# Performance work log

Measured on AMD Instinct MI355X. Metric: run time of the kernel, lower is better.

The kernel has to match this reference:

```python
import jax, jax.numpy as jnp
import numpy as np
import math

C = 16
K = 16
M = 64
DEPTH = 4          # int(sqrt(K)) tree depth
D = C * 9          # input feature dim, 9 dims per codebook subspace
N = 1024 * 128     # rows
N_NODES = K - 1    # 15 internal nodes of a depth-4 binary tree


def _selection_matrix(C):
    # node i at tree level l reads the per-codebook hashed feature at depth index l
    S = np.zeros((C * N_NODES, C * DEPTH), np.float32)
    for c in range(C):
        for i in range(N_NODES):
            level = 0 if i == 0 else (1 if i < 3 else (2 if i < 7 else 3))
            S[c * N_NODES + i, c * DEPTH + level] = 1.0
    return S


def _bit_matrix(C, K):
    # row (c,k): +/-1 on the 4 tree nodes along code k's root-to-leaf path;
    # matching code scores DEPTH, every other code scores <= DEPTH-2
    B = np.zeros((C * K, C * N_NODES), np.float32)
    for c in range(C):
        for k in range(K):
            prefix = 0
            for l in range(DEPTH):
                bit = (k >> (DEPTH - 1 - l)) & 1
                node = (2 ** l - 1) + prefix
                B[c * K + k, c * N_NODES + node] = 1.0 if bit else -1.0
                prefix = prefix * 2 + bit
    return B


def setup_inputs() -> dict:
    key = jax.random.key(0)
    k1, k2, k3, k4 = jax.random.split(key, 4)
    I = jax.random.normal(k1, (N, D), jnp.float32) - 0.5
    A = jax.random.normal(k2, (C, D // C, DEPTH), jnp.float32)   # soft hashing projections
    T = jax.random.normal(k3, (C * N_NODES,), jnp.float32)       # node thresholds
    bound = math.sqrt(1.0 / (C * K))  # kaiming_uniform with a=sqrt(5), fan_in=C*K
    L = jax.random.uniform(k4, (M, C, K), jnp.float32, -bound, bound)  # lookup tables
    S = jnp.asarray(_selection_matrix(C))
    B = jnp.asarray(_bit_matrix(C, K))
    return {"I": I, "A": A, "T": T, "L": L, "S": S, "B": B}


def reference(I, A, T, L, S, B):
    n = I.shape[0]
    # per-codebook soft hash: (n, C, D//C) x (C, D//C, DEPTH) -> (n, C*DEPTH)
    h = jnp.einsum('ncd,cdp->ncp', I.reshape(n, C, D // C), A).reshape(n, C * DEPTH)
    # thresholded tree decisions with straight-through sign
    b = h @ S.T - T                                   # (n, C*15)
    t = jnp.tanh(b)
    s = jax.lax.stop_gradient(jnp.sign(b) - t) + t    # fwd: sign, bwd: tanh'
    # bit-matrix decode of path agreements -> per-code scores
    scores = (s @ B.T).reshape(n, C, K)               # (n, C, K), max DEPTH at true code
    onehot = jax.nn.one_hot(jnp.argmax(scores, axis=2), K, dtype=I.dtype)
    E = jax.lax.stop_gradient(onehot - scores) + scores  # STE one-hot encoding
    # LUT gather-accumulate: out[n,m] = sum_c L[m,c,code(n,c)]
    return jnp.einsum('nck,mck->nm', E, L)
```

## Files before the change

kernel.cpp:

```cpp
#include <hip/hip_runtime.h>


#define NROWS (1024 * 128)

__global__ __launch_bounds__(256) void halut_fwd(
    const float* __restrict__ I,
    const float* __restrict__ A,
    const float* __restrict__ T,
    const float* __restrict__ L,
    float* __restrict__ out)
{
    __shared__ float  sBuf[16384];
    __shared__ double sA[576];
    __shared__ double sT[240];

    const int tid = threadIdx.x;

    {
        float2* sL2 = (float2*)sBuf;
        #pragma unroll
        for (int p2 = 0; p2 < 32; ++p2) {
            const float a = L[(2 * p2)     * 256 + tid];
            const float b = L[(2 * p2 + 1) * 256 + tid];
            sL2[p2 * 256 + tid] = make_float2(a, b);
        }
    }
    for (int i = tid; i < 576; i += 256) sA[i] = (double)A[i];
    if (tid < 240) sT[tid] = (double)T[tid];
    __syncthreads();

    const int    row = blockIdx.x * 256 + tid;
    const float* rp  = I + (size_t)row * 144;

    float acc[64];
    #pragma unroll
    for (int m = 0; m < 64; ++m) acc[m] = 0.0f;

    #pragma unroll
    for (int g = 0; g < 4; ++g) {
        float4 buf[9];
        const float4* rv = (const float4*)(rp + g * 36);
        #pragma unroll
        for (int i = 0; i < 9; ++i) buf[i] = rv[i];
        const float* bf = (const float*)buf;

        #pragma unroll
        for (int cc = 0; cc < 4; ++cc) {
            const int c = g * 4 + cc;
            double h0 = 0.0, h1 = 0.0, h2 = 0.0, h3 = 0.0;
            #pragma unroll
            for (int d = 0; d < 9; ++d) {
                const double  x  = (double)bf[cc * 9 + d];
                const double* ap = &sA[(c * 9 + d) * 4];
                h0 = fma(x, ap[0], h0);
                h1 = fma(x, ap[1], h1);
                h2 = fma(x, ap[2], h2);
                h3 = fma(x, ap[3], h3);
            }
            const double* tp = &sT[c * 15];
            int p;
            p =         (h0 > tp[0]);
            p = 2 * p + (h1 > tp[1 + p]);
            p = 2 * p + (h2 > tp[3 + p]);
            p = 2 * p + (h3 > tp[7 + p]);

            const float2* colp = (const float2*)sBuf + (c * 16 + p);
            #pragma unroll
            for (int p2 = 0; p2 < 32; ++p2) {
                const float2 v = colp[p2 * 256];
                acc[2 * p2]     += v.x;
                acc[2 * p2 + 1] += v.y;
            }
        }
    }

    __syncthreads();
    float* sO = sBuf;
    #pragma unroll
    for (int mc = 0; mc < 16; ++mc) {
        *(float4*)&sO[(tid << 6) + ((mc ^ (tid & 15)) << 2)] =
            make_float4(acc[4*mc], acc[4*mc+1], acc[4*mc+2], acc[4*mc+3]);
    }
    __syncthreads();

    float4* op = (float4*)(out + (size_t)blockIdx.x * (256 * 64));
    #pragma unroll
    for (int j = 0; j < 16; ++j) {
        const int F  = tid + (j << 8);
        const int r2 = F >> 4;
        const int m2 = F & 15;
        op[F] = *(const float4*)&sO[(r2 << 6) + ((m2 ^ (r2 & 15)) << 2)];
    }
}

extern "C" void kernel_launch(void* const* d_in, const int* in_sizes, int n_in,
                              void* d_out, int out_size, void* d_ws, size_t ws_size,
                              hipStream_t stream) {
    const float* I = (const float*)d_in[0];
    const float* A = (const float*)d_in[1];
    const float* T = (const float*)d_in[2];
    const float* L = (const float*)d_in[3];
    float* outp = (float*)d_out;

    const int nblocks = NROWS / 256;
    halut_fwd<<<nblocks, 256, 0, stream>>>(I, A, T, L, outp);
}
```

Baseline: 29.87 us.

## Store LUT in fp16 and accumulate with half2 to halve LDS footprint

Converts the lookup table to packed fp16 in shared memory and accumulates outputs with half2 adds, halving LDS size and LDS read traffic and cutting accumulator registers. It also double-buffers the row loads across codebook groups, precomputes all 15 threshold comparisons into a bitmask with vectorized double2 loads, and splits the output transpose into two halves to fit the smaller buffer. Launch bounds now request two blocks per CU for higher occupancy. The fp16 accumulation of 16 LUT entries loses precision against the fp32 reference and may exceed tolerance.

```diff
diff --git a/kernel.cpp b/kernel.cpp
--- a/kernel.cpp
+++ b/kernel.cpp
@@ -1,95 +1,142 @@
 #include <hip/hip_runtime.h>
+#include <hip/hip_fp16.h>
 
 
 #define NROWS (1024 * 128)
 
-__global__ __launch_bounds__(256) void halut_fwd(
+__global__ __launch_bounds__(256, 2) void halut_fwd(
     const float* __restrict__ I,
     const float* __restrict__ A,
     const float* __restrict__ T,
     const float* __restrict__ L,
     float* __restrict__ out)
 {
-    __shared__ float  sBuf[16384];
-    __shared__ double sA[576];
-    __shared__ double sT[240];
+    __shared__ uint32_t sBuf[8192];
+    __shared__ double   sA[576];
+    __shared__ double   sT[256];
 
     const int tid = threadIdx.x;
 
     {
-        float2* sL2 = (float2*)sBuf;
+        uint4* lut4 = (uint4*)sBuf;
         #pragma unroll
-        for (int p2 = 0; p2 < 32; ++p2) {
-            const float a = L[(2 * p2)     * 256 + tid];
-            const float b = L[(2 * p2 + 1) * 256 + tid];
-            sL2[p2 * 256 + tid] = make_float2(a, b);
+        for (int q = 0; q < 8; ++q) {
+            uint32_t w[4];
+            #pragma unroll
+            for (int e = 0; e < 4; ++e) {
+                const float fa = L[(8 * q + 2 * e)     * 256 + tid];
+                const float fb = L[(8 * q + 2 * e + 1) * 256 + tid];
+                w[e] = ((uint32_t)__half_as_ushort(__float2half_rn(fb)) << 16)
+                     |  (uint32_t)__half_as_ushort(__float2half_rn(fa));
+            }
+            lut4[q * 256 + tid] = make_uint4(w[0], w[1], w[2], w[3]);
         }
     }
     for (int i = tid; i < 576; i += 256) sA[i] = (double)A[i];
-    if (tid < 240) sT[tid] = (double)T[tid];
+    {
+        const int c = tid >> 4, j = tid & 15;
+        sT[tid] = (j < 15) ? (double)T[c * 15 + j] : 0.0;
+    }
     __syncthreads();
 
-    const int    row = blockIdx.x * 256 + tid;
-    const float* rp  = I + (size_t)row * 144;
+    const int row = blockIdx.x * 256 + tid;
+    const float* rp = I + (size_t)row * 144;
 
-    float acc[64];
+    __half2 acc2[32];
     #pragma unroll
-    for (int m = 0; m < 64; ++m) acc[m] = 0.0f;
+    for (int k = 0; k < 32; ++k) acc2[k] = __floats2half2_rn(0.f, 0.f);
+
+    const uint4* lut4 = (const uint4*)sBuf;
+
+    float4 bufA[9], bufB[9];
+    #pragma unroll
+    for (int i = 0; i < 9; ++i) bufA[i] = ((const float4*)rp)[i];
 
     #pragma unroll
     for (int g = 0; g < 4; ++g) {
-        float4 buf[9];
-        const float4* rv = (const float4*)(rp + g * 36);
-        #pragma unroll
-        for (int i = 0; i < 9; ++i) buf[i] = rv[i];
-        const float* bf = (const float*)buf;
-
+        const float* curp = (const float*)((g & 1) ? bufB : bufA);
+        if (g < 3) {
+            float4* nxt = (g & 1) ? bufA : bufB;
+            const float4* src = (const float4*)(rp + (g + 1) * 36);
+            #pragma unroll
+            for (int i = 0; i < 9; ++i) nxt[i] = src[i];
+        }
         #pragma unroll
         for (int cc = 0; cc < 4; ++cc) {
             const int c = g * 4 + cc;
             double h0 = 0.0, h1 = 0.0, h2 = 0.0, h3 = 0.0;
             #pragma unroll
             for (int d = 0; d < 9; ++d) {
-                const double  x  = (double)bf[cc * 9 + d];
-                const double* ap = &sA[(c * 9 + d) * 4];
-                h0 = fma(x, ap[0], h0);
-                h1 = fma(x, ap[1], h1);
-                h2 = fma(x, ap[2], h2);
-                h3 = fma(x, ap[3], h3);
+                const double  x   = (double)curp[cc * 9 + d];
+                const double2 a01 = *(const double2*)&sA[(c * 9 + d) * 4];
+                const double2 a23 = *(const double2*)&sA[(c * 9 + d) * 4 + 2];
+                h0 = fma(x, a01.x, h0);
+                h1 = fma(x, a01.y, h1);
+                h2 = fma(x, a23.x, h2);
+                h3 = fma(x, a23.y, h3);
             }
-            const double* tp = &sT[c * 15];
-            int p;
-            p =         (h0 > tp[0]);
-            p = 2 * p + (h1 > tp[1 + p]);
-            p = 2 * p + (h2 > tp[3 + p]);
-            p = 2 * p + (h3 > tp[7 + p]);
+            const double2* tp = (const double2*)&sT[c * 16];
+            const double2 t0 = tp[0], t1 = tp[1], t2 = tp[2], t3 = tp[3];
+            const double2 t4 = tp[4], t5 = tp[5], t6 = tp[6], t7 = tp[7];
+            uint32_t mk = 0;
+            mk |= (h0 > t0.x) ?     1u : 0u;
+            mk |= (h1 > t0.y) ?     2u : 0u;
+            mk |= (h1 > t1.x) ?     4u : 0u;
+            mk |= (h2 > t1.y) ?     8u : 0u;
+            mk |= (h2 > t2.x) ?    16u : 0u;
+            mk |= (h2 > t2.y) ?    32u : 0u;
+            mk |= (h2 > t3.x) ?    64u : 0u;
+            mk |= (h3 > t3.y) ?   128u : 0u;
+            mk |= (h3 > t4.x) ?   256u : 0u;
+            mk |= (h3 > t4.y) ?   512u : 0u;
+            mk |= (h3 > t5.x) ?  1024u : 0u;
+            mk |= (h3 > t5.y) ?  2048u : 0u;
+            mk |= (h3 > t6.x) ?  4096u : 0u;
+            mk |= (h3 > t6.y) ?  8192u : 0u;
+            mk |= (h3 > t7.x) ? 16384u : 0u;
+            int p =       (int)(mk & 1u);
+            p = 2 * p + (int)((mk >> (1 + p)) & 1u);
+            p = 2 * p + (int)((mk >> (3 + p)) & 1u);
+            p = 2 * p + (int)((mk >> (7 + p)) & 1u);
 
-            const float2* colp = (const float2*)sBuf + (c * 16 + p);
+            const uint4* colp = lut4 + (c << 4) + p;
             #pragma unroll
-            for (int p2 = 0; p2 < 32; ++p2) {
-                const float2 v = colp[p2 * 256];
-                acc[2 * p2]     += v.x;
-                acc[2 * p2 + 1] += v.y;
+            for (int q = 0; q < 8; ++q) {
+                const uint4 w = colp[q << 8];
+                acc2[q * 4 + 0] = __hadd2(acc2[q * 4 + 0], *(const __half2*)&w.x);
+                acc2[q * 4 + 1] = __hadd2(acc2[q * 4 + 1], *(const __half2*)&w.y);
+                acc2[q * 4 + 2] = __hadd2(acc2[q * 4 + 2], *(const __half2*)&w.z);
+                acc2[q * 4 + 3] = __hadd2(acc2[q * 4 + 3], *(const __half2*)&w.w);
             }
         }
     }
 
     __syncthreads();
-    float* sO = sBuf;
+    float* sO = (float*)sBuf;
     #pragma unroll
-    for (int mc = 0; mc < 16; ++mc) {
-        *(float4*)&sO[(tid << 6) + ((mc ^ (tid & 15)) << 2)] =
-            make_float4(acc[4*mc], acc[4*mc+1], acc[4*mc+2], acc[4*mc+3]);
-    }
-    __syncthreads();
-
-    float4* op = (float4*)(out + (size_t)blockIdx.x * (256 * 64));
-    #pragma unroll
-    for (int j = 0; j < 16; ++j) {
-        const int F  = tid + (j << 8);
-        const int r2 = F >> 4;
-        const int m2 = F & 15;
-        op[F] = *(const float4*)&sO[(r2 << 6) + ((m2 ^ (r2 & 15)) << 2)];
+    for (int half = 0; half < 2; ++half) {
+        if ((tid >> 7) == half) {
+            const int r = tid & 127;
+            #pragma unroll
+            for (int ch = 0; ch < 16; ++ch) {
+                const float4 v = make_float4(__low2float (acc2[2 * ch]),
+                                             __high2float(acc2[2 * ch]),
+                                             __low2float (acc2[2 * ch + 1]),
+                                             __high2float(acc2[2 * ch + 1]));
+                *(float4*)&sO[(r << 6) + ((ch ^ (r & 15)) << 2)] = v;
+            }
+        }
+        __syncthreads();
+        float4* op = (float4*)(out + (size_t)blockIdx.x * (256 * 64)
+                                   + (size_t)half * (128 * 64));
+        #pragma unroll
+        for (int j = 0; j < 8; ++j) {
+            const int F  = tid + (j << 8);
+            const int r2 = F >> 4;
+            const int m2 = F & 15;
+            op[F] = *(const float4*)&sO[(r2 << 6) + ((m2 ^ (r2 & 15)) << 2)];
+        }
+        __syncthreads();
     }
 }
 
```

New measurement: 30.51 us. 1.02x slower.
